# Optimization experiments

Hardware: AMD Instinct MI355X
Metric: run time of the kernel (lower is better)

## Reference

```python
import jax, jax.numpy as jnp
import numpy as np
import math

H_DIM = 512
QKV_DIM = 512
NUM_HEADS = 8
HEAD_DIM = QKV_DIM // NUM_HEADS
B, S = 4, 8192


def setup_inputs() -> dict:
    key = jax.random.key(0)
    ks = jax.random.split(key, 9)
    sc = 1.0 / math.sqrt(H_DIM)
    return {
        "x": jax.random.normal(ks[0], (B, S, H_DIM), dtype=jnp.float32),
        "Wq": jax.random.normal(ks[1], (QKV_DIM, H_DIM), dtype=jnp.float32) * sc,
        "bq": jax.random.normal(ks[2], (QKV_DIM,), dtype=jnp.float32) * 0.01,
        "Wk": jax.random.normal(ks[3], (QKV_DIM, H_DIM), dtype=jnp.float32) * sc,
        "bk": jax.random.normal(ks[4], (QKV_DIM,), dtype=jnp.float32) * 0.01,
        "Wv": jax.random.normal(ks[5], (QKV_DIM, H_DIM), dtype=jnp.float32) * sc,
        "bv": jax.random.normal(ks[6], (QKV_DIM,), dtype=jnp.float32) * 0.01,
        "Wl": jax.random.normal(ks[7], (H_DIM, QKV_DIM), dtype=jnp.float32) * sc,
        "bl": jax.random.normal(ks[8], (H_DIM,), dtype=jnp.float32) * 0.01,
    }


def _split_heads(t):
    # [B, S, QKV] -> [B, num_heads, S, head_dim]
    Bn, Sn, _ = t.shape
    return t.reshape(Bn, Sn, NUM_HEADS, HEAD_DIM).transpose(0, 2, 1, 3)


def reference(x, Wq, bq, Wk, bk, Wv, bv, Wl, bl):
    # self-attention: k = v = q = x
    q = _split_heads(x @ Wq.T + bq)
    k = _split_heads(x @ Wk.T + bk)
    v = _split_heads(x @ Wv.T + bv)
    seq_len = q.shape[2]
    # kv: [B, H, head_dim, head_dim] -- tiny intermediate, scaled by 1/sqrt(S)
    kv = jnp.einsum('bhsd,bhse->bhde', k, v) * (1.0 / math.sqrt(seq_len))
    # dropout_rate = 0.0 -> identity
    out = jnp.einsum('bhsd,bhde->bhse', q, kv)  # [B, H, S, head_dim]
    out = out.transpose(0, 2, 1, 3).reshape(x.shape[0], seq_len, QKV_DIM)
    return out @ Wl.T + bl
```

## Files before the change

kernel.cpp:

```cpp
#include <hip/hip_runtime.h>
#include <hip/hip_bf16.h>

#define DEVI __device__ __forceinline__

typedef __bf16 bf16x8 __attribute__((ext_vector_type(8)));
typedef __bf16 bf16x4 __attribute__((ext_vector_type(4)));
typedef float  f32x4  __attribute__((ext_vector_type(4)));

constexpr int Bn = 4, Sn = 8192, Hn = 512;
constexpr float INV_SQRT_S = 0.011048543456039806f;

#define GLOAD16(gp, lp) __builtin_amdgcn_global_load_lds(                      \
    (const __attribute__((address_space(1))) unsigned int*)(gp),               \
    (__attribute__((address_space(3))) unsigned int*)(lp), 16, 0, 0)

DEVI void split2(float v, __bf16* h, __bf16* l) {
  __bf16 hh = (__bf16)v; *h = hh; *l = (__bf16)(v - (float)hh);
}

__global__ __launch_bounds__(256) void k0_split(const float* __restrict__ x,
    __bf16* __restrict__ xh, __bf16* __restrict__ xl,
    __bf16* __restrict__ xhT, __bf16* __restrict__ xlT, float* __restrict__ ssum)
{
  __shared__ __bf16 lh[64*68], ll[64*68];
  __shared__ float csum[64];
  int wg = blockIdx.x;
  int ct = wg & 7, st = (wg >> 3) & 127, b = wg >> 10;
  int s0 = st * 64, c0 = ct * 64;
  int t = threadIdx.x, r0 = t >> 4, c4 = t & 15;
  if (t < 64) csum[t] = 0.f;
  __syncthreads();
  float sloc[4] = {0.f, 0.f, 0.f, 0.f};
#pragma unroll
  for (int i = 0; i < 4; ++i) {
    int r = r0 + 16 * i;
    size_t base = ((size_t)(b * Sn + s0 + r)) * Hn + c0 + c4 * 4;
    float4 v = *(const float4*)(x + base);
    __bf16 h[4], l[4];
    split2(v.x, &h[0], &l[0]); split2(v.y, &h[1], &l[1]);
    split2(v.z, &h[2], &l[2]); split2(v.w, &h[3], &l[3]);
    *(bf16x4*)(xh + base) = (bf16x4){h[0], h[1], h[2], h[3]};
    *(bf16x4*)(xl + base) = (bf16x4){l[0], l[1], l[2], l[3]};
#pragma unroll
    for (int j = 0; j < 4; ++j) {
      lh[(c4 * 4 + j) * 68 + r] = h[j];
      ll[(c4 * 4 + j) * 68 + r] = l[j];
    }
    sloc[0] += v.x; sloc[1] += v.y; sloc[2] += v.z; sloc[3] += v.w;
  }
#pragma unroll
  for (int j = 0; j < 4; ++j) atomicAdd(&csum[c4 * 4 + j], sloc[j]);
  __syncthreads();
#pragma unroll
  for (int i = 0; i < 4; ++i) {
    int cr = r0 + 16 * i;
    size_t tb = ((size_t)(b * Hn + c0 + cr)) * Sn + s0 + c4 * 4;
    *(bf16x4*)(xhT + tb) = *(const bf16x4*)(lh + cr * 68 + c4 * 4);
    *(bf16x4*)(xlT + tb) = *(const bf16x4*)(ll + cr * 68 + c4 * 4);
  }
  if (t < 64) atomicAdd(&ssum[b * Hn + c0 + t], csum[t]);
}

__global__ __launch_bounds__(256) void k0w_weights(
    const float* __restrict__ Wq, const float* __restrict__ Wk,
    const float* __restrict__ Wv, const float* __restrict__ Wl,
    __bf16* WqTh, __bf16* WqTl, __bf16* Wkh, __bf16* Wkl,
    __bf16* Wvh, __bf16* Wvl, __bf16* Wlh, __bf16* Wll)
{
  __shared__ __bf16 lh[64*68], ll[64*68];
  int wg = blockIdx.x;
  int ct = wg & 7, st = (wg >> 3) & 7, arr = wg >> 6;
  int t = threadIdx.x, r0 = t >> 4, c4 = t & 15;
  int rbase = st * 64, cbase = ct * 64;
  const float* src = (arr == 0) ? Wk : (arr == 1) ? Wv : (arr == 2) ? Wl : Wq;
  __bf16* dh = (arr == 0) ? Wkh : (arr == 1) ? Wvh : Wlh;
  __bf16* dl = (arr == 0) ? Wkl : (arr == 1) ? Wvl : Wll;
#pragma unroll
  for (int i = 0; i < 4; ++i) {
    int r = r0 + 16 * i;
    size_t base = ((size_t)(rbase + r)) * 512 + cbase + c4 * 4;
    float4 v = *(const float4*)(src + base);
    __bf16 h[4], l[4];
    split2(v.x, &h[0], &l[0]); split2(v.y, &h[1], &l[1]);
    split2(v.z, &h[2], &l[2]); split2(v.w, &h[3], &l[3]);
    if (arr < 3) {
      *(bf16x4*)(dh + base) = (bf16x4){h[0], h[1], h[2], h[3]};
      *(bf16x4*)(dl + base) = (bf16x4){l[0], l[1], l[2], l[3]};
    } else {
#pragma unroll
      for (int j = 0; j < 4; ++j) {
        lh[(c4 * 4 + j) * 68 + r] = h[j];
        ll[(c4 * 4 + j) * 68 + r] = l[j];
      }
    }
  }
  if (arr == 3) {
    __syncthreads();
#pragma unroll
    for (int i = 0; i < 4; ++i) {
      int cr = r0 + 16 * i;
      size_t tb = ((size_t)(cbase + cr)) * 512 + rbase + c4 * 4;
      *(bf16x4*)(WqTh + tb) = *(const bf16x4*)(lh + cr * 68 + c4 * 4);
      *(bf16x4*)(WqTl + tb) = *(const bf16x4*)(ll + cr * 68 + c4 * 4);
    }
  }
}

DEVI void stage128(const __bf16* src, int ld, __bf16* dst, int wave, int lane) {
#pragma unroll
  for (int i = 0; i < 4; ++i) {
    int g = i * 256 + wave * 64 + lane;
    int row = g >> 3, kk = (g & 7) * 8;
    GLOAD16(src + (size_t)row * ld + kk, dst + (size_t)(i * 256 + wave * 64) * 8);
  }
}

DEVI void frag_compute128(const __bf16* As, const __bf16* Bs, int lane, int wr, int wc,
                          f32x4 acc[4][4]) {
#pragma unroll
  for (int kk = 0; kk < 64; kk += 32) {
    bf16x8 a[4], bb[4];
#pragma unroll
    for (int mf = 0; mf < 4; ++mf)
      a[mf] = *(const bf16x8*)(As + (size_t)(wr * 64 + mf * 16 + (lane & 15)) * 64 + kk + (lane >> 4) * 8);
#pragma unroll
    for (int nf = 0; nf < 4; ++nf)
      bb[nf] = *(const bf16x8*)(Bs + (size_t)(wc * 64 + nf * 16 + (lane & 15)) * 64 + kk + (lane >> 4) * 8);
#pragma unroll
    for (int mf = 0; mf < 4; ++mf)
#pragma unroll
      for (int nf = 0; nf < 4; ++nf)
        acc[mf][nf] = __builtin_amdgcn_mfma_f32_16x16x32_bf16(a[mf], bb[nf], acc[mf][nf], 0, 0, 0);
  }
}

__global__ __launch_bounds__(256) void k1_pr(const __bf16* __restrict__ xhT,
                                             const __bf16* __restrict__ xlT,
                                             float* __restrict__ PR)
{
  __shared__ alignas(16) __bf16 lds[2][2][128 * 64];
  int wg = blockIdx.x;
  int kc = wg & 3, nt = (wg >> 2) & 7, mt = (wg >> 5) & 3, b = wg >> 7;
  int t = threadIdx.x, wave = t >> 6, lane = t & 63, wr = wave >> 1, wc = wave & 1;
  const __bf16* A = xhT + ((size_t)(b * Hn + mt * 128)) * Sn;
  const __bf16* Bp = (nt < 4) ? xhT + ((size_t)(b * Hn + nt * 128)) * Sn
                              : xlT + ((size_t)(b * Hn + (nt - 4) * 128)) * Sn;
  int k0 = kc * 2048;
  f32x4 acc[4][4];
#pragma unroll
  for (int mf = 0; mf < 4; ++mf)
#pragma unroll
    for (int nf = 0; nf < 4; ++nf)
#pragma unroll
      for (int r = 0; r < 4; ++r) acc[mf][nf][r] = 0.f;

  stage128(A + k0, Sn, lds[0][0], wave, lane);
  stage128(Bp + k0, Sn, lds[0][1], wave, lane);
  __syncthreads();
  for (int st = 0; st < 32; ++st) {
    int cur = st & 1;
    if (st < 31) {
      stage128(A + k0 + (st + 1) * 64, Sn, lds[1 - cur][0], wave, lane);
      stage128(Bp + k0 + (st + 1) * 64, Sn, lds[1 - cur][1], wave, lane);
    }
    frag_compute128(lds[cur][0], lds[cur][1], lane, wr, wc, acc);
    __syncthreads();
  }
#pragma unroll
  for (int mf = 0; mf < 4; ++mf)
#pragma unroll
    for (int nf = 0; nf < 4; ++nf) {
      int m = mt * 128 + wr * 64 + mf * 16 + (lane >> 4) * 4;
      int n = nt * 128 + wc * 64 + nf * 16 + (lane & 15);
      float* dst = PR + ((size_t)(b * Hn) + m) * 1024 + n;
#pragma unroll
      for (int r = 0; r < 4; ++r) atomicAdd(dst + (size_t)r * 1024, acc[mf][nf][r]);
    }
}

__global__ __launch_bounds__(256) void k2a_gasm(const float* __restrict__ PR,
                                                __bf16* __restrict__ Gh, __bf16* __restrict__ Gl)
{
  __shared__ float tr[64 * 68];
  int wg = blockIdx.x;
  int qt = wg & 7, pt = (wg >> 3) & 7, b = wg >> 6;
  int p0 = pt * 64, q0 = qt * 64;
  int t = threadIdx.x, r0 = t >> 4, c4 = t & 15;
#pragma unroll
  for (int i = 0; i < 4; ++i) {
    int rr = r0 + 16 * i, cc = c4 * 4;
    float4 v = *(const float4*)(PR + ((size_t)(b * 512) + q0 + rr) * 1024 + 512 + p0 + cc);
    tr[(cc + 0) * 68 + rr] = v.x; tr[(cc + 1) * 68 + rr] = v.y;
    tr[(cc + 2) * 68 + rr] = v.z; tr[(cc + 3) * 68 + rr] = v.w;
  }
  __syncthreads();
#pragma unroll
  for (int i = 0; i < 4; ++i) {
    int r = r0 + 16 * i, c = c4 * 4;
    size_t rb = ((size_t)(b * 512) + p0 + r) * 1024;
    float4 P4 = *(const float4*)(PR + rb + q0 + c);
    float4 R4 = *(const float4*)(PR + rb + 512 + q0 + c);
    float g[4] = {P4.x + R4.x + tr[r * 68 + c + 0], P4.y + R4.y + tr[r * 68 + c + 1],
                  P4.z + R4.z + tr[r * 68 + c + 2], P4.w + R4.w + tr[r * 68 + c + 3]};
    __bf16 h[4], l[4];
#pragma unroll
    for (int j = 0; j < 4; ++j) split2(g[j], &h[j], &l[j]);
    size_t o = ((size_t)(b * 512) + p0 + r) * 512 + q0 + c;
    *(bf16x4*)(Gh + o) = (bf16x4){h[0], h[1], h[2], h[3]};
    *(bf16x4*)(Gl + o) = (bf16x4){l[0], l[1], l[2], l[3]};
  }
}

DEVI void stage64(const __bf16* src, int ld, __bf16* dst, int wave, int lane) {
#pragma unroll
  for (int i = 0; i < 2; ++i) {
    int g = i * 256 + wave * 64 + lane;
    int row = g >> 3, kk = (g & 7) * 8;
    GLOAD16(src + (size_t)row * ld + kk, dst + (size_t)(i * 256 + wave * 64) * 8);
  }
}

DEVI void gemm3_64(const __bf16* Ah, const __bf16* Al, int lda,
                   const __bf16* Bh, const __bf16* Bl, int ldb,
                   int K, __bf16* lds, int t, f32x4 acc[2][2])
{
  int wave = t >> 6, lane = t & 63, wr = wave >> 1, wc = wave & 1;
#pragma unroll
  for (int mf = 0; mf < 2; ++mf)
#pragma unroll
    for (int nf = 0; nf < 2; ++nf)
#pragma unroll
      for (int r = 0; r < 4; ++r) acc[mf][nf][r] = 0.f;
  for (int ks = 0; ks < K; ks += 64) {
    stage64(Ah + ks, lda, lds + 0 * 4096, wave, lane);
    stage64(Al + ks, lda, lds + 1 * 4096, wave, lane);
    stage64(Bh + ks, ldb, lds + 2 * 4096, wave, lane);
    stage64(Bl + ks, ldb, lds + 3 * 4096, wave, lane);
    __syncthreads();
#pragma unroll
    for (int kk = 0; kk < 64; kk += 32) {
      bf16x8 ah[2], al[2], bh[2], bl[2];
#pragma unroll
      for (int mf = 0; mf < 2; ++mf) {
        int ro = (wr * 32 + mf * 16 + (lane & 15)) * 64 + kk + (lane >> 4) * 8;
        ah[mf] = *(const bf16x8*)(lds + 0 * 4096 + ro);
        al[mf] = *(const bf16x8*)(lds + 1 * 4096 + ro);
      }
#pragma unroll
      for (int nf = 0; nf < 2; ++nf) {
        int ro = (wc * 32 + nf * 16 + (lane & 15)) * 64 + kk + (lane >> 4) * 8;
        bh[nf] = *(const bf16x8*)(lds + 2 * 4096 + ro);
        bl[nf] = *(const bf16x8*)(lds + 3 * 4096 + ro);
      }
#pragma unroll
      for (int mf = 0; mf < 2; ++mf)
#pragma unroll
        for (int nf = 0; nf < 2; ++nf) {
          acc[mf][nf] = __builtin_amdgcn_mfma_f32_16x16x32_bf16(ah[mf], bh[nf], acc[mf][nf], 0, 0, 0);
          acc[mf][nf] = __builtin_amdgcn_mfma_f32_16x16x32_bf16(ah[mf], bl[nf], acc[mf][nf], 0, 0, 0);
          acc[mf][nf] = __builtin_amdgcn_mfma_f32_16x16x32_bf16(al[mf], bh[nf], acc[mf][nf], 0, 0, 0);
        }
    }
    __syncthreads();
  }
}

__global__ __launch_bounds__(256) void k2t(const __bf16* Wkh, const __bf16* Wkl,
                                           const __bf16* Gh, const __bf16* Gl,
                                           __bf16* Th, __bf16* Tl)
{
  __shared__ alignas(16) __bf16 lds[4 * 4096];
  int wg = blockIdx.x;
  int nt = wg & 7, mt = (wg >> 3) & 7, b = wg >> 6;
  int t = threadIdx.x;
  f32x4 acc[2][2];
  gemm3_64(Wkh + (size_t)(mt * 64) * 512, Wkl + (size_t)(mt * 64) * 512, 512,
           Gh + ((size_t)(b * 512 + nt * 64)) * 512, Gl + ((size_t)(b * 512 + nt * 64)) * 512, 512,
           512, lds, t, acc);
  int wave = t >> 6, lane = t & 63, wr = wave >> 1, wc = wave & 1;
#pragma unroll
  for (int mf = 0; mf < 2; ++mf)
#pragma unroll
    for (int nf = 0; nf < 2; ++nf)
#pragma unroll
      for (int r = 0; r < 4; ++r) {
        int m = mt * 64 + wr * 32 + mf * 16 + (lane >> 4) * 4 + r;
        int n = nt * 64 + wc * 32 + nf * 16 + (lane & 15);
        __bf16 h, l; split2(acc[mf][nf][r], &h, &l);
        size_t o = ((size_t)(b * 512) + m) * 512 + n;
        Th[o] = h; Tl[o] = l;
      }
}

__global__ __launch_bounds__(256) void k2kv(const __bf16* Th, const __bf16* Tl,
                                            const __bf16* Wvh, const __bf16* Wvl, float* kvf)
{
  __shared__ alignas(16) __bf16 lds[4 * 4096];
  int wg = blockIdx.x;
  int kc = wg & 3, h = (wg >> 2) & 7, b = wg >> 5;
  int t = threadIdx.x;
  f32x4 acc[2][2];
  gemm3_64(Th + ((size_t)(b * 512 + h * 64)) * 512 + kc * 128,
           Tl + ((size_t)(b * 512 + h * 64)) * 512 + kc * 128, 512,
           Wvh + (size_t)(h * 64) * 512 + kc * 128,
           Wvl + (size_t)(h * 64) * 512 + kc * 128, 512, 128, lds, t, acc);
  int wave = t >> 6, lane = t & 63, wr = wave >> 1, wc = wave & 1;
#pragma unroll
  for (int mf = 0; mf < 2; ++mf)
#pragma unroll
    for (int nf = 0; nf < 2; ++nf)
#pragma unroll
      for (int r = 0; r < 4; ++r) {
        int m = wr * 32 + mf * 16 + (lane >> 4) * 4 + r;
        int n = wc * 32 + nf * 16 + (lane & 15);
        atomicAdd(&kvf[(((size_t)b * 8 + h) * 64 + m) * 64 + n], acc[mf][nf][r]);
      }
}

__global__ __launch_bounds__(64) void k2kvpack(const float* kvf, const float* ssum,
    const float* Wk, const float* Wv, const float* bq, const float* bk, const float* bv,
    __bf16* kvTh, __bf16* kvTl, float* bqkv)
{
  __shared__ float kvl[64 * 65];
  __shared__ float wks[64], wvs[64];
  int wg = blockIdx.x;
  int h = wg & 7, b = wg >> 3;
  int d = threadIdx.x;
  const float* sb = ssum + b * 512;
  const float* wkrow = Wk + (size_t)(h * 64 + d) * 512;
  const float* wvrow = Wv + (size_t)(h * 64 + d) * 512;
  float t1 = 0.f, t2 = 0.f;
  for (int p = 0; p < 512; ++p) { t1 += wkrow[p] * sb[p]; t2 += wvrow[p] * sb[p]; }
  wks[d] = t1; wvs[d] = t2;
  __syncthreads();
  float bkd = bk[h * 64 + d];
  for (int e = 0; e < 64; ++e) {
    float v = kvf[(((size_t)b * 8 + h) * 64 + d) * 64 + e];
    float bve = bv[h * 64 + e];
    v += wks[d] * bve + bkd * wvs[e] + 8192.0f * bkd * bve;
    kvl[d * 65 + e] = v * INV_SQRT_S;
  }
  __syncthreads();
  int e = d;
  float acc = 0.f;
  for (int dd = 0; dd < 64; ++dd) acc += bq[h * 64 + dd] * kvl[dd * 65 + e];
  bqkv[b * 512 + h * 64 + e] = acc;
  for (int dd = 0; dd < 64; ++dd) {
    __bf16 hh, ll; split2(kvl[dd * 65 + e], &hh, &ll);
    size_t o = (((size_t)b * 8 + h) * 64 + e) * 64 + dd;
    kvTh[o] = hh; kvTl[o] = ll;
  }
}

__global__ __launch_bounds__(256) void k2u(const __bf16* WqTh, const __bf16* WqTl,
                                           const __bf16* kvTh, const __bf16* kvTl,
                                           __bf16* Uh, __bf16* Ul)
{
  __shared__ alignas(16) __bf16 lds[4 * 4096];
  int wg = blockIdx.x;
  int ib = wg & 7, h = (wg >> 3) & 7, b = wg >> 6;
  int t = threadIdx.x;
  f32x4 acc[2][2];
  gemm3_64(WqTh + (size_t)(ib * 64) * 512 + h * 64,
           WqTl + (size_t)(ib * 64) * 512 + h * 64, 512,
           kvTh + ((size_t)b * 8 + h) * 4096,
           kvTl + ((size_t)b * 8 + h) * 4096, 64, 64, lds, t, acc);
  int wave = t >> 6, lane = t & 63, wr = wave >> 1, wc = wave & 1;
#pragma unroll
  for (int mf = 0; mf < 2; ++mf)
#pragma unroll
    for (int nf = 0; nf < 2; ++nf)
#pragma unroll
      for (int r = 0; r < 4; ++r) {
        int m = ib * 64 + wr * 32 + mf * 16 + (lane >> 4) * 4 + r;
        int n = h * 64 + wc * 32 + nf * 16 + (lane & 15);
        __bf16 hh, ll; split2(acc[mf][nf][r], &hh, &ll);
        size_t o = ((size_t)(b * 512) + m) * 512 + n;
        Uh[o] = hh; Ul[o] = ll;
      }
}

__global__ __launch_bounds__(256) void k2weff(const __bf16* Uh, const __bf16* Ul,
                                              const __bf16* Wlh, const __bf16* Wll,
                                              __bf16* WTh, __bf16* WTl)
{
  __shared__ alignas(16) __bf16 lds[4 * 4096];
  __shared__ float trf[64 * 68];
  int wg = blockIdx.x;
  int jb = wg & 7, ib = (wg >> 3) & 7, b = wg >> 6;
  int t = threadIdx.x;
  f32x4 acc[2][2];
  gemm3_64(Uh + ((size_t)(b * 512 + ib * 64)) * 512,
           Ul + ((size_t)(b * 512 + ib * 64)) * 512, 512,
           Wlh + (size_t)(jb * 64) * 512, Wll + (size_t)(jb * 64) * 512, 512,
           512, lds, t, acc);
  int wave = t >> 6, lane = t & 63, wr = wave >> 1, wc = wave & 1;
#pragma unroll
  for (int mf = 0; mf < 2; ++mf)
#pragma unroll
    for (int nf = 0; nf < 2; ++nf)
#pragma unroll
      for (int r = 0; r < 4; ++r) {
        int m = wr * 32 + mf * 16 + (lane >> 4) * 4 + r;
        int n = wc * 32 + nf * 16 + (lane & 15);
        trf[m * 68 + n] = acc[mf][nf][r];
      }
  __syncthreads();
  int n_ = t >> 2, mseg = (t & 3) * 16;
  size_t rowbase = ((size_t)(b * 512 + jb * 64 + n_)) * 512 + ib * 64 + mseg;
#pragma unroll
  for (int q = 0; q < 16; ++q) {
    __bf16 hh, ll; split2(trf[(mseg + q) * 68 + n_], &hh, &ll);
    WTh[rowbase + q] = hh; WTl[rowbase + q] = ll;
  }
}

__global__ __launch_bounds__(512) void k2beff(const float* bqkv, const float* Wl,
                                              const float* bl, float* beff)
{
  __shared__ float bq_s[512];
  int b = blockIdx.x, j = threadIdx.x;
  bq_s[j] = bqkv[b * 512 + j];
  __syncthreads();
  const float4* wrow = (const float4*)(Wl + (size_t)j * 512);
  float acc = bl[j];
  for (int m4 = 0; m4 < 128; ++m4) {
    float4 w = wrow[m4];
    acc += w.x * bq_s[m4 * 4] + w.y * bq_s[m4 * 4 + 1] + w.z * bq_s[m4 * 4 + 2] + w.w * bq_s[m4 * 4 + 3];
  }
  beff[b * 512 + j] = acc;
}

__global__ __launch_bounds__(256) void k3_final(const __bf16* __restrict__ xh,
    const __bf16* __restrict__ xl, const __bf16* __restrict__ WTh,
    const __bf16* __restrict__ WTl, const float* __restrict__ beff,
    float* __restrict__ out)
{
  __shared__ alignas(16) __bf16 lds[2][2][128 * 64];
  int wg = blockIdx.x;
  int nt = wg & 3, mt = (wg >> 2) & 63, b = wg >> 8;
  int t = threadIdx.x, wave = t >> 6, lane = t & 63, wr = wave >> 1, wc = wave & 1;
  const __bf16* Axh = xh + ((size_t)(b * Sn + mt * 128)) * Hn;
  const __bf16* Axl = xl + ((size_t)(b * Sn + mt * 128)) * Hn;
  const __bf16* Bh = WTh + ((size_t)(b * Hn + nt * 128)) * Hn;
  const __bf16* Bl = WTl + ((size_t)(b * Hn + nt * 128)) * Hn;
  f32x4 acc[4][4];
#pragma unroll
  for (int mf = 0; mf < 4; ++mf)
#pragma unroll
    for (int nf = 0; nf < 4; ++nf)
#pragma unroll
      for (int r = 0; r < 4; ++r) acc[mf][nf][r] = 0.f;

  stage128(Axh, Hn, lds[0][0], wave, lane);
  stage128(Bh, Hn, lds[0][1], wave, lane);
  __syncthreads();
  for (int st = 0; st < 24; ++st) {
    int cur = st & 1;
    if (st < 23) {
      int nst = st + 1, term = nst >> 3, kcol = (nst & 7) * 64;
      const __bf16* As = (term == 2) ? Axl : Axh;
      const __bf16* Bs = (term == 1) ? Bl : Bh;
      stage128(As + kcol, Hn, lds[1 - cur][0], wave, lane);
      stage128(Bs + kcol, Hn, lds[1 - cur][1], wave, lane);
    }
    frag_compute128(lds[cur][0], lds[cur][1], lane, wr, wc, acc);
    __syncthreads();
  }
#pragma unroll
  for (int mf = 0; mf < 4; ++mf)
#pragma unroll
    for (int nf = 0; nf < 4; ++nf) {
      int n = nt * 128 + wc * 64 + nf * 16 + (lane & 15);
      float be = beff[b * Hn + n];
      int m0 = mt * 128 + wr * 64 + mf * 16 + (lane >> 4) * 4;
#pragma unroll
      for (int r = 0; r < 4; ++r)
        out[((size_t)(b * Sn) + m0 + r) * Hn + n] = acc[mf][nf][r] + be;
    }
}

extern "C" void kernel_launch(void* const* d_in, const int* in_sizes, int n_in,
                              void* d_out, int out_size, void* d_ws, size_t ws_size,
                              hipStream_t stream)
{
  (void)in_sizes; (void)n_in; (void)out_size; (void)ws_size;
  const float* x  = (const float*)d_in[0];
  const float* Wq = (const float*)d_in[1];
  const float* bq = (const float*)d_in[2];
  const float* Wk = (const float*)d_in[3];
  const float* bk = (const float*)d_in[4];
  const float* Wv = (const float*)d_in[5];
  const float* bv = (const float*)d_in[6];
  const float* Wl = (const float*)d_in[7];
  const float* bl = (const float*)d_in[8];
  float* out = (float*)d_out;

  char* p = (char*)d_ws;
  auto alloc = [&](size_t bytes) { char* r = p; p += (bytes + 255) & ~(size_t)255; return r; };
  const size_t XB = (size_t)Bn * Sn * Hn * 2;
  __bf16* xh  = (__bf16*)alloc(XB);
  __bf16* xl  = (__bf16*)alloc(XB);
  __bf16* xhT = (__bf16*)alloc(XB);
  __bf16* xlT = (__bf16*)alloc(XB);
  float*  PR  = (float*)alloc((size_t)Bn * 512 * 1024 * 4);
  float*  ssum = (float*)alloc((size_t)Bn * 512 * 4);
  __bf16* Gh = (__bf16*)alloc((size_t)Bn * 512 * 512 * 2);
  __bf16* Gl = (__bf16*)alloc((size_t)Bn * 512 * 512 * 2);
  const size_t WB = 512 * 512 * 2;
  __bf16* WqTh = (__bf16*)alloc(WB); __bf16* WqTl = (__bf16*)alloc(WB);
  __bf16* Wkh  = (__bf16*)alloc(WB); __bf16* Wkl  = (__bf16*)alloc(WB);
  __bf16* Wvh  = (__bf16*)alloc(WB); __bf16* Wvl  = (__bf16*)alloc(WB);
  __bf16* Wlh  = (__bf16*)alloc(WB); __bf16* Wll  = (__bf16*)alloc(WB);
  __bf16* Th = (__bf16*)alloc((size_t)Bn * 512 * 512 * 2);
  __bf16* Tl = (__bf16*)alloc((size_t)Bn * 512 * 512 * 2);
  float*  kvf = (float*)alloc((size_t)Bn * 8 * 64 * 64 * 4);
  __bf16* kvTh = (__bf16*)alloc((size_t)Bn * 8 * 64 * 64 * 2);
  __bf16* kvTl = (__bf16*)alloc((size_t)Bn * 8 * 64 * 64 * 2);
  float*  bqkv = (float*)alloc((size_t)Bn * 512 * 4);
  __bf16* Uh = (__bf16*)alloc((size_t)Bn * 512 * 512 * 2);
  __bf16* Ul = (__bf16*)alloc((size_t)Bn * 512 * 512 * 2);
  __bf16* WTh = (__bf16*)alloc((size_t)Bn * 512 * 512 * 2);
  __bf16* WTl = (__bf16*)alloc((size_t)Bn * 512 * 512 * 2);
  float*  beff = (float*)alloc((size_t)Bn * 512 * 4);

  hipMemsetAsync(PR, 0, (size_t)Bn * 512 * 1024 * 4, stream);
  hipMemsetAsync(ssum, 0, (size_t)Bn * 512 * 4, stream);
  hipMemsetAsync(kvf, 0, (size_t)Bn * 8 * 64 * 64 * 4, stream);

  k0_split<<<4096, 256, 0, stream>>>(x, xh, xl, xhT, xlT, ssum);
  k0w_weights<<<256, 256, 0, stream>>>(Wq, Wk, Wv, Wl, WqTh, WqTl, Wkh, Wkl, Wvh, Wvl, Wlh, Wll);
  k1_pr<<<512, 256, 0, stream>>>(xhT, xlT, PR);
  k2a_gasm<<<256, 256, 0, stream>>>(PR, Gh, Gl);
  k2t<<<256, 256, 0, stream>>>(Wkh, Wkl, Gh, Gl, Th, Tl);
  k2kv<<<128, 256, 0, stream>>>(Th, Tl, Wvh, Wvl, kvf);
  k2kvpack<<<32, 64, 0, stream>>>(kvf, ssum, Wk, Wv, bq, bk, bv, kvTh, kvTl, bqkv);
  k2u<<<256, 256, 0, stream>>>(WqTh, WqTl, kvTh, kvTl, Uh, Ul);
  k2weff<<<256, 256, 0, stream>>>(Uh, Ul, Wlh, Wll, WTh, WTl);
  k2beff<<<4, 512, 0, stream>>>(bqkv, Wl, bl, beff);
  k3_final<<<1024, 256, 0, stream>>>(xh, xl, WTh, WTl, beff, out);
}
```

Baseline: 391.0 us.

## Replace atomic split-K with slabs, reorder kv chain, swizzle blocks

k1_pr now writes each K-chunk's partial Gram matrix to its own slab instead of using float atomics, and k2a_gasm sums the four slabs; this removes the PR memset and the atomic traffic. The kv computation is reassociated as Wk·(G·Wv^T) per head, which replaces the k2t/k2kv/k2kvpack chain (full 512x512 T product, atomics, a 64-thread pack kernel) with a per-head GW product and a fused kv kernel that also does the bias and sum reductions with 256 threads. Block indices in k1_pr and k3_final are remapped so that blocks landing on the same XCD share inputs, stores are vectorised to bf16x8, and intermediate buffers are aliased onto the dead xhT region. The costs are 4x the PR memory traffic in the reduce kernel and a changed accumulation order.

After: 360.1 us. 7.9% less time.

```diff
diff --git a/kernel.cpp b/kernel.cpp
--- a/kernel.cpp
+++ b/kernel.cpp
@@ -139,8 +139,9 @@
                                              float* __restrict__ PR)
 {
   __shared__ alignas(16) __bf16 lds[2][2][128 * 64];
-  int wg = blockIdx.x;
-  int kc = wg & 3, nt = (wg >> 2) & 7, mt = (wg >> 5) & 3, b = wg >> 7;
+  int bid = blockIdx.x;
+  int wgid = (bid & 7) * 64 + (bid >> 3);
+  int nt = wgid & 7, mt = (wgid >> 3) & 3, kc = (wgid >> 5) & 3, b = wgid >> 7;
   int t = threadIdx.x, wave = t >> 6, lane = t & 63, wr = wave >> 1, wc = wave & 1;
   const __bf16* A = xhT + ((size_t)(b * Hn + mt * 128)) * Sn;
   const __bf16* Bp = (nt < 4) ? xhT + ((size_t)(b * Hn + nt * 128)) * Sn
@@ -172,9 +173,9 @@
     for (int nf = 0; nf < 4; ++nf) {
       int m = mt * 128 + wr * 64 + mf * 16 + (lane >> 4) * 4;
       int n = nt * 128 + wc * 64 + nf * 16 + (lane & 15);
-      float* dst = PR + ((size_t)(b * Hn) + m) * 1024 + n;
-#pragma unroll
-      for (int r = 0; r < 4; ++r) atomicAdd(dst + (size_t)r * 1024, acc[mf][nf][r]);
+      float* dst = PR + (((size_t)kc * 4 + b) * 512 + m) * 1024 + n;
+#pragma unroll
+      for (int r = 0; r < 4; ++r) dst[(size_t)r * 1024] = acc[mf][nf][r];
     }
 }
 
@@ -182,6 +183,7 @@
                                                 __bf16* __restrict__ Gh, __bf16* __restrict__ Gl)
 {
   __shared__ float tr[64 * 68];
+  constexpr size_t SLAB = (size_t)4 * 512 * 1024;
   int wg = blockIdx.x;
   int qt = wg & 7, pt = (wg >> 3) & 7, b = wg >> 6;
   int p0 = pt * 64, q0 = qt * 64;
@@ -189,7 +191,13 @@
 #pragma unroll
   for (int i = 0; i < 4; ++i) {
     int rr = r0 + 16 * i, cc = c4 * 4;
-    float4 v = *(const float4*)(PR + ((size_t)(b * 512) + q0 + rr) * 1024 + 512 + p0 + cc);
+    size_t off = ((size_t)(b * 512) + q0 + rr) * 1024 + 512 + p0 + cc;
+    float4 v = {0.f, 0.f, 0.f, 0.f};
+#pragma unroll
+    for (int kc = 0; kc < 4; ++kc) {
+      float4 u = *(const float4*)(PR + kc * SLAB + off);
+      v.x += u.x; v.y += u.y; v.z += u.z; v.w += u.w;
+    }
     tr[(cc + 0) * 68 + rr] = v.x; tr[(cc + 1) * 68 + rr] = v.y;
     tr[(cc + 2) * 68 + rr] = v.z; tr[(cc + 3) * 68 + rr] = v.w;
   }
@@ -198,8 +206,14 @@
   for (int i = 0; i < 4; ++i) {
     int r = r0 + 16 * i, c = c4 * 4;
     size_t rb = ((size_t)(b * 512) + p0 + r) * 1024;
-    float4 P4 = *(const float4*)(PR + rb + q0 + c);
-    float4 R4 = *(const float4*)(PR + rb + 512 + q0 + c);
+    float4 P4 = {0.f, 0.f, 0.f, 0.f}, R4 = {0.f, 0.f, 0.f, 0.f};
+#pragma unroll
+    for (int kc = 0; kc < 4; ++kc) {
+      float4 u = *(const float4*)(PR + kc * SLAB + rb + q0 + c);
+      float4 w = *(const float4*)(PR + kc * SLAB + rb + 512 + q0 + c);
+      P4.x += u.x; P4.y += u.y; P4.z += u.z; P4.w += u.w;
+      R4.x += w.x; R4.y += w.y; R4.z += w.z; R4.w += w.w;
+    }
     float g[4] = {P4.x + R4.x + tr[r * 68 + c + 0], P4.y + R4.y + tr[r * 68 + c + 1],
                   P4.z + R4.z + tr[r * 68 + c + 2], P4.w + R4.w + tr[r * 68 + c + 3]};
     __bf16 h[4], l[4];
@@ -265,45 +279,20 @@
   }
 }
 
-__global__ __launch_bounds__(256) void k2t(const __bf16* Wkh, const __bf16* Wkl,
-                                           const __bf16* Gh, const __bf16* Gl,
-                                           __bf16* Th, __bf16* Tl)
+__global__ __launch_bounds__(256) void kA_gw(const __bf16* Gh, const __bf16* Gl,
+                                             const __bf16* Wvh, const __bf16* Wvl,
+                                             __bf16* GWTh, __bf16* GWTl)
 {
   __shared__ alignas(16) __bf16 lds[4 * 4096];
+  __shared__ float trf[64 * 68];
   int wg = blockIdx.x;
-  int nt = wg & 7, mt = (wg >> 3) & 7, b = wg >> 6;
+  int pt = wg & 7, h = (wg >> 3) & 7, b = wg >> 6;
   int t = threadIdx.x;
   f32x4 acc[2][2];
-  gemm3_64(Wkh + (size_t)(mt * 64) * 512, Wkl + (size_t)(mt * 64) * 512, 512,
-           Gh + ((size_t)(b * 512 + nt * 64)) * 512, Gl + ((size_t)(b * 512 + nt * 64)) * 512, 512,
+  gemm3_64(Gh + ((size_t)(b * 512 + pt * 64)) * 512,
+           Gl + ((size_t)(b * 512 + pt * 64)) * 512, 512,
+           Wvh + (size_t)(h * 64) * 512, Wvl + (size_t)(h * 64) * 512, 512,
            512, lds, t, acc);
-  int wave = t >> 6, lane = t & 63, wr = wave >> 1, wc = wave & 1;
-#pragma unroll
-  for (int mf = 0; mf < 2; ++mf)
-#pragma unroll
-    for (int nf = 0; nf < 2; ++nf)
-#pragma unroll
-      for (int r = 0; r < 4; ++r) {
-        int m = mt * 64 + wr * 32 + mf * 16 + (lane >> 4) * 4 + r;
-        int n = nt * 64 + wc * 32 + nf * 16 + (lane & 15);
-        __bf16 h, l; split2(acc[mf][nf][r], &h, &l);
-        size_t o = ((size_t)(b * 512) + m) * 512 + n;
-        Th[o] = h; Tl[o] = l;
-      }
-}
-
-__global__ __launch_bounds__(256) void k2kv(const __bf16* Th, const __bf16* Tl,
-                                            const __bf16* Wvh, const __bf16* Wvl, float* kvf)
-{
-  __shared__ alignas(16) __bf16 lds[4 * 4096];
-  int wg = blockIdx.x;
-  int kc = wg & 3, h = (wg >> 2) & 7, b = wg >> 5;
-  int t = threadIdx.x;
-  f32x4 acc[2][2];
-  gemm3_64(Th + ((size_t)(b * 512 + h * 64)) * 512 + kc * 128,
-           Tl + ((size_t)(b * 512 + h * 64)) * 512 + kc * 128, 512,
-           Wvh + (size_t)(h * 64) * 512 + kc * 128,
-           Wvl + (size_t)(h * 64) * 512 + kc * 128, 512, 128, lds, t, acc);
   int wave = t >> 6, lane = t & 63, wr = wave >> 1, wc = wave & 1;
 #pragma unroll
   for (int mf = 0; mf < 2; ++mf)
@@ -313,42 +302,113 @@
       for (int r = 0; r < 4; ++r) {
         int m = wr * 32 + mf * 16 + (lane >> 4) * 4 + r;
         int n = wc * 32 + nf * 16 + (lane & 15);
-        atomicAdd(&kvf[(((size_t)b * 8 + h) * 64 + m) * 64 + n], acc[mf][nf][r]);
-      }
-}
-
-__global__ __launch_bounds__(64) void k2kvpack(const float* kvf, const float* ssum,
-    const float* Wk, const float* Wv, const float* bq, const float* bk, const float* bv,
+        trf[m * 68 + n] = acc[mf][nf][r];
+      }
+  __syncthreads();
+  int e_ = t >> 2, pseg = (t & 3) * 16;
+  size_t rowbase = (((size_t)b * 8 + h) * 64 + e_) * 512 + pt * 64 + pseg;
+#pragma unroll
+  for (int seg = 0; seg < 2; ++seg) {
+    bf16x8 vh, vl;
+#pragma unroll
+    for (int j = 0; j < 8; ++j) {
+      __bf16 hh, ll; split2(trf[(pseg + seg * 8 + j) * 68 + e_], &hh, &ll);
+      vh[j] = hh; vl[j] = ll;
+    }
+    *(bf16x8*)(GWTh + rowbase + seg * 8) = vh;
+    *(bf16x8*)(GWTl + rowbase + seg * 8) = vl;
+  }
+}
+
+__global__ __launch_bounds__(256) void kB_kv(const __bf16* Wkh, const __bf16* Wkl,
+    const __bf16* GWTh, const __bf16* GWTl,
+    const float* __restrict__ Wk, const float* __restrict__ Wv,
+    const float* __restrict__ ssum, const float* __restrict__ bq,
+    const float* __restrict__ bk, const float* __restrict__ bv,
     __bf16* kvTh, __bf16* kvTl, float* bqkv)
 {
+  __shared__ alignas(16) __bf16 lds[4 * 4096];
   __shared__ float kvl[64 * 65];
-  __shared__ float wks[64], wvs[64];
+  __shared__ float wks[64], wvs[64], red[256];
   int wg = blockIdx.x;
   int h = wg & 7, b = wg >> 3;
-  int d = threadIdx.x;
-  const float* sb = ssum + b * 512;
-  const float* wkrow = Wk + (size_t)(h * 64 + d) * 512;
-  const float* wvrow = Wv + (size_t)(h * 64 + d) * 512;
-  float t1 = 0.f, t2 = 0.f;
-  for (int p = 0; p < 512; ++p) { t1 += wkrow[p] * sb[p]; t2 += wvrow[p] * sb[p]; }
-  wks[d] = t1; wvs[d] = t2;
-  __syncthreads();
-  float bkd = bk[h * 64 + d];
-  for (int e = 0; e < 64; ++e) {
-    float v = kvf[(((size_t)b * 8 + h) * 64 + d) * 64 + e];
-    float bve = bv[h * 64 + e];
-    v += wks[d] * bve + bkd * wvs[e] + 8192.0f * bkd * bve;
-    kvl[d * 65 + e] = v * INV_SQRT_S;
-  }
-  __syncthreads();
-  int e = d;
-  float acc = 0.f;
-  for (int dd = 0; dd < 64; ++dd) acc += bq[h * 64 + dd] * kvl[dd * 65 + e];
-  bqkv[b * 512 + h * 64 + e] = acc;
-  for (int dd = 0; dd < 64; ++dd) {
-    __bf16 hh, ll; split2(kvl[dd * 65 + e], &hh, &ll);
-    size_t o = (((size_t)b * 8 + h) * 64 + e) * 64 + dd;
-    kvTh[o] = hh; kvTl[o] = ll;
+  int t = threadIdx.x;
+  f32x4 acc[2][2];
+  gemm3_64(Wkh + (size_t)(h * 64) * 512, Wkl + (size_t)(h * 64) * 512, 512,
+           GWTh + ((size_t)b * 8 + h) * 64 * 512,
+           GWTl + ((size_t)b * 8 + h) * 64 * 512, 512,
+           512, lds, t, acc);
+  int wave = t >> 6, lane = t & 63, wr = wave >> 1, wc = wave & 1;
+#pragma unroll
+  for (int mf = 0; mf < 2; ++mf)
+#pragma unroll
+    for (int nf = 0; nf < 2; ++nf)
+#pragma unroll
+      for (int r = 0; r < 4; ++r) {
+        int m = wr * 32 + mf * 16 + (lane >> 4) * 4 + r;
+        int n = wc * 32 + nf * 16 + (lane & 15);
+        kvl[m * 65 + n] = acc[mf][nf][r];
+      }
+  int row = t & 63, part = t >> 6;
+  const float* sb = ssum + b * 512 + part * 128;
+  {
+    const float4* wr4 = (const float4*)(Wk + (size_t)(h * 64 + row) * 512 + part * 128);
+    float p1 = 0.f;
+#pragma unroll
+    for (int i = 0; i < 32; ++i) {
+      float4 w = wr4[i];
+      p1 += w.x * sb[i * 4] + w.y * sb[i * 4 + 1] + w.z * sb[i * 4 + 2] + w.w * sb[i * 4 + 3];
+    }
+    red[t] = p1;
+  }
+  __syncthreads();
+  if (t < 64) wks[t] = red[t] + red[t + 64] + red[t + 128] + red[t + 192];
+  __syncthreads();
+  {
+    const float4* wr4 = (const float4*)(Wv + (size_t)(h * 64 + row) * 512 + part * 128);
+    float p1 = 0.f;
+#pragma unroll
+    for (int i = 0; i < 32; ++i) {
+      float4 w = wr4[i];
+      p1 += w.x * sb[i * 4] + w.y * sb[i * 4 + 1] + w.z * sb[i * 4 + 2] + w.w * sb[i * 4 + 3];
+    }
+    red[t] = p1;
+  }
+  __syncthreads();
+  if (t < 64) wvs[t] = red[t] + red[t + 64] + red[t + 128] + red[t + 192];
+  __syncthreads();
+  {
+    int d = t >> 2, eseg = (t & 3) * 16;
+    float bkd = bk[h * 64 + d], wksd = wks[d];
+#pragma unroll
+    for (int j = 0; j < 16; ++j) {
+      int e = eseg + j;
+      float bve = bv[h * 64 + e];
+      float v = kvl[d * 65 + e] + wksd * bve + bkd * wvs[e] + 8192.0f * bkd * bve;
+      kvl[d * 65 + e] = v * INV_SQRT_S;
+    }
+  }
+  __syncthreads();
+  if (t < 64) {
+    int e = t;
+    float a2 = 0.f;
+    for (int dd = 0; dd < 64; ++dd) a2 += bq[h * 64 + dd] * kvl[dd * 65 + e];
+    bqkv[b * 512 + h * 64 + e] = a2;
+  }
+  {
+    int e = t >> 2, dseg = (t & 3) * 16;
+    size_t rowbase = (((size_t)b * 8 + h) * 64 + e) * 64 + dseg;
+#pragma unroll
+    for (int seg = 0; seg < 2; ++seg) {
+      bf16x8 vh, vl;
+#pragma unroll
+      for (int j = 0; j < 8; ++j) {
+        __bf16 hh, ll; split2(kvl[(dseg + seg * 8 + j) * 65 + e], &hh, &ll);
+        vh[j] = hh; vl[j] = ll;
+      }
+      *(bf16x8*)(kvTh + rowbase + seg * 8) = vh;
+      *(bf16x8*)(kvTl + rowbase + seg * 8) = vl;
+    }
   }
 }
 
@@ -409,9 +469,15 @@
   int n_ = t >> 2, mseg = (t & 3) * 16;
   size_t rowbase = ((size_t)(b * 512 + jb * 64 + n_)) * 512 + ib * 64 + mseg;
 #pragma unroll
-  for (int q = 0; q < 16; ++q) {
-    __bf16 hh, ll; split2(trf[(mseg + q) * 68 + n_], &hh, &ll);
-    WTh[rowbase + q] = hh; WTl[rowbase + q] = ll;
+  for (int seg = 0; seg < 2; ++seg) {
+    bf16x8 vh, vl;
+#pragma unroll
+    for (int j = 0; j < 8; ++j) {
+      __bf16 hh, ll; split2(trf[(mseg + seg * 8 + j) * 68 + n_], &hh, &ll);
+      vh[j] = hh; vl[j] = ll;
+    }
+    *(bf16x8*)(WTh + rowbase + seg * 8) = vh;
+    *(bf16x8*)(WTl + rowbase + seg * 8) = vl;
   }
 }
 
@@ -437,8 +503,9 @@
     float* __restrict__ out)
 {
   __shared__ alignas(16) __bf16 lds[2][2][128 * 64];
-  int wg = blockIdx.x;
-  int nt = wg & 3, mt = (wg >> 2) & 63, b = wg >> 8;
+  int bid = blockIdx.x;
+  int wgid = (bid & 7) * 128 + (bid >> 3);
+  int nt = wgid & 3, mt = (wgid >> 2) & 63, b = wgid >> 8;
   int t = threadIdx.x, wave = t >> 6, lane = t & 63, wr = wave >> 1, wc = wave & 1;
   const __bf16* Axh = xh + ((size_t)(b * Sn + mt * 128)) * Hn;
   const __bf16* Axl = xl + ((size_t)(b * Sn + mt * 128)) * Hn;
@@ -503,38 +570,37 @@
   __bf16* xl  = (__bf16*)alloc(XB);
   __bf16* xhT = (__bf16*)alloc(XB);
   __bf16* xlT = (__bf16*)alloc(XB);
-  float*  PR  = (float*)alloc((size_t)Bn * 512 * 1024 * 4);
+  float*  PR  = (float*)alloc((size_t)4 * Bn * 512 * 1024 * 4);
   float*  ssum = (float*)alloc((size_t)Bn * 512 * 4);
-  __bf16* Gh = (__bf16*)alloc((size_t)Bn * 512 * 512 * 2);
-  __bf16* Gl = (__bf16*)alloc((size_t)Bn * 512 * 512 * 2);
   const size_t WB = 512 * 512 * 2;
   __bf16* WqTh = (__bf16*)alloc(WB); __bf16* WqTl = (__bf16*)alloc(WB);
   __bf16* Wkh  = (__bf16*)alloc(WB); __bf16* Wkl  = (__bf16*)alloc(WB);
   __bf16* Wvh  = (__bf16*)alloc(WB); __bf16* Wvl  = (__bf16*)alloc(WB);
   __bf16* Wlh  = (__bf16*)alloc(WB); __bf16* Wll  = (__bf16*)alloc(WB);
-  __bf16* Th = (__bf16*)alloc((size_t)Bn * 512 * 512 * 2);
-  __bf16* Tl = (__bf16*)alloc((size_t)Bn * 512 * 512 * 2);
-  float*  kvf = (float*)alloc((size_t)Bn * 8 * 64 * 64 * 4);
-  __bf16* kvTh = (__bf16*)alloc((size_t)Bn * 8 * 64 * 64 * 2);
-  __bf16* kvTl = (__bf16*)alloc((size_t)Bn * 8 * 64 * 64 * 2);
   float*  bqkv = (float*)alloc((size_t)Bn * 512 * 4);
-  __bf16* Uh = (__bf16*)alloc((size_t)Bn * 512 * 512 * 2);
-  __bf16* Ul = (__bf16*)alloc((size_t)Bn * 512 * 512 * 2);
-  __bf16* WTh = (__bf16*)alloc((size_t)Bn * 512 * 512 * 2);
-  __bf16* WTl = (__bf16*)alloc((size_t)Bn * 512 * 512 * 2);
   float*  beff = (float*)alloc((size_t)Bn * 512 * 4);
 
-  hipMemsetAsync(PR, 0, (size_t)Bn * 512 * 1024 * 4, stream);
+  char* q = (char*)xhT;
+  auto alloc2 = [&](size_t bytes) { char* r = q; q += (bytes + 255) & ~(size_t)255; return r; };
+  __bf16* Gh   = (__bf16*)alloc2((size_t)Bn * 512 * 512 * 2);
+  __bf16* Gl   = (__bf16*)alloc2((size_t)Bn * 512 * 512 * 2);
+  __bf16* GWTh = (__bf16*)alloc2((size_t)Bn * 8 * 64 * 512 * 2);
+  __bf16* GWTl = (__bf16*)alloc2((size_t)Bn * 8 * 64 * 512 * 2);
+  __bf16* kvTh = (__bf16*)alloc2((size_t)Bn * 8 * 64 * 64 * 2);
+  __bf16* kvTl = (__bf16*)alloc2((size_t)Bn * 8 * 64 * 64 * 2);
+  __bf16* Uh   = (__bf16*)alloc2((size_t)Bn * 512 * 512 * 2);
+  __bf16* Ul   = (__bf16*)alloc2((size_t)Bn * 512 * 512 * 2);
+  __bf16* WTh  = (__bf16*)alloc2((size_t)Bn * 512 * 512 * 2);
+  __bf16* WTl  = (__bf16*)alloc2((size_t)Bn * 512 * 512 * 2);
+
   hipMemsetAsync(ssum, 0, (size_t)Bn * 512 * 4, stream);
-  hipMemsetAsync(kvf, 0, (size_t)Bn * 8 * 64 * 64 * 4, stream);
 
   k0_split<<<4096, 256, 0, stream>>>(x, xh, xl, xhT, xlT, ssum);
   k0w_weights<<<256, 256, 0, stream>>>(Wq, Wk, Wv, Wl, WqTh, WqTl, Wkh, Wkl, Wvh, Wvl, Wlh, Wll);
   k1_pr<<<512, 256, 0, stream>>>(xhT, xlT, PR);
   k2a_gasm<<<256, 256, 0, stream>>>(PR, Gh, Gl);
-  k2t<<<256, 256, 0, stream>>>(Wkh, Wkl, Gh, Gl, Th, Tl);
-  k2kv<<<128, 256, 0, stream>>>(Th, Tl, Wvh, Wvl, kvf);
-  k2kvpack<<<32, 64, 0, stream>>>(kvf, ssum, Wk, Wv, bq, bk, bv, kvTh, kvTl, bqkv);
+  kA_gw<<<256, 256, 0, stream>>>(Gh, Gl, Wvh, Wvl, GWTh, GWTl);
+  kB_kv<<<32, 256, 0, stream>>>(Wkh, Wkl, GWTh, GWTl, Wk, Wv, ssum, bq, bk, bv, kvTh, kvTl, bqkv);
   k2u<<<256, 256, 0, stream>>>(WqTh, WqTl, kvTh, kvTl, Uh, Ul);
   k2weff<<<256, 256, 0, stream>>>(Uh, Ul, Wlh, Wll, WTh, WTl);
   k2beff<<<4, 512, 0, stream>>>(bqkv, Wl, bl, beff);
```
